# Optimization experiments

Measured on AMD Instinct MI355X. Metric: run time of the kernel, lower is better.

The kernel has to match this reference:

```python
import jax, jax.numpy as jnp
import numpy as np

B, T, D, H = 4, 256, 256, 4
D2 = 2 * D
DH = D2 // H
SCALE = float(D) ** -0.5


def _swish(x):
    return x * jax.nn.sigmoid(x)


def setup_inputs():
    key = jax.random.key(0)
    ks = jax.random.split(key, 16)

    def w(k, shape, fan_in):
        return jax.random.normal(k, shape, dtype=jnp.float32) / np.float32(np.sqrt(fan_in))

    return {
        "x": jax.random.normal(ks[0], (B, T, D), dtype=jnp.float32),
        "ln_g": jnp.ones((D,), jnp.float32), "ln_b": jnp.zeros((D,), jnp.float32),
        "W_left": w(ks[1], (D2, D), D), "b_left": jnp.zeros((D2,), jnp.float32),
        "W_right": w(ks[2], (D2, D), D), "b_right": jnp.zeros((D2,), jnp.float32),
        "Wi": w(ks[3], (1, D2), D2), "bi": jnp.zeros((1,), jnp.float32),
        "Wf": w(ks[4], (1, D2), D2), "bf": jnp.zeros((1,), jnp.float32),
        "Wo": w(ks[5], (D2, D2), D2), "bo": jnp.zeros((D2,), jnp.float32),
        "Wq": w(ks[6], (H, DH, DH), DH),
        "Wk": w(ks[7], (H, DH, DH), DH),
        "Wv": w(ks[8], (H, DH, DH), DH),
        "conv_w": w(ks[9], (D2, D2, 4), D2 * 4), "conv_b": jnp.zeros((D2,), jnp.float32),
        "skip_W": w(ks[10], (D2, D2), D2),
        "gn_g": jnp.ones((D2,), jnp.float32), "gn_b": jnp.zeros((D2,), jnp.float32),
        "W_last": w(ks[11], (D, D2), D2), "b_last": jnp.zeros((D,), jnp.float32),
    }


def reference(x, ln_g, ln_b, W_left, b_left, W_right, b_right, Wi, bi, Wf, bf,
              Wo, bo, Wq, Wk, Wv, conv_w, conv_b, skip_W, gn_g, gn_b, W_last, b_last):
    # LayerNorm over last dim (eps=1e-5, torch default)
    mu = x.mean(-1, keepdims=True)
    var = x.var(-1, keepdims=True)
    x_norm = (x - mu) * jax.lax.rsqrt(var + 1e-5) * ln_g + ln_b

    x_left = x_norm @ W_left.T + b_left          # (B,T,D2)
    x_right = x_norm @ W_right.T + b_right       # (B,T,D2)

    # causal conv1d: kernel 4, left pad 3
    xc = jnp.transpose(x_left, (0, 2, 1))        # (B,C,T)
    yc = jax.lax.conv_general_dilated(xc, conv_w, (1,), [(3, 0)],
                                      dimension_numbers=("NCH", "OIH", "NCH"))
    x_trans = _swish(jnp.transpose(yc + conv_b[None, :, None], (0, 2, 1)))  # (B,T,D2)

    def bd(z, W):  # block-diagonal linear, W: (H, out_h, in_h)
        zr = z.reshape(B, T, H, DH)
        return jnp.einsum("bthi,hoi->btho", zr, W).reshape(B, T, D2)

    # precompute all per-step projections (hoist GEMMs out of the scan)
    i_bar = x_left @ Wi.T + bi                   # (B,T,1)
    f_bar = x_left @ Wf.T + bf                   # (B,T,1)
    o = jax.nn.sigmoid(x_left @ Wo.T + bo)       # (B,T,D2)
    q = bd(x_trans, Wq)
    k = SCALE * bd(x_trans, Wk)
    v = bd(x_left, Wv)

    xs = tuple(jnp.swapaxes(a, 0, 1) for a in (i_bar, f_bar, q, k, v))  # (T,B,...)
    c0 = jnp.zeros((B, D2, D2), x.dtype)
    n0 = jnp.zeros((B, D2), x.dtype)
    m0 = jnp.zeros((B, 1), x.dtype)

    def step(carry, xs_t):
        c, n, m = carry
        ib, fb, qt, kt, vt = xs_t
        m_next = jnp.maximum(fb + m, ib)
        i_g = jnp.exp(ib - m_next)               # (B,1)
        f_g = jnp.exp(fb + m - m_next)           # (B,1)
        c_next = f_g[..., None] * c + i_g[..., None] * (vt[:, :, None] * kt[:, None, :])
        n_next = f_g * n + i_g * kt
        cq = jnp.einsum("bde,be->bd", c_next, qt)
        denom = jnp.maximum(jnp.abs(jnp.sum(n_next * qt, -1, keepdims=True)), 1.0)
        return (c_next, n_next, m_next), cq / (denom + 1e-8)

    _, h_bar = jax.lax.scan(step, (c0, n0, m0), xs)
    h_seq = o * jnp.swapaxes(h_bar, 0, 1)        # (B,T,D2), output gate applied per step

    # GroupNorm on (B, C, T): normalize per (batch, group) over C/G and T
    z = h_seq.reshape(B, T, H, DH)
    mu_g = z.mean(axis=(1, 3), keepdims=True)
    var_g = z.var(axis=(1, 3), keepdims=True)
    zn = ((z - mu_g) * jax.lax.rsqrt(var_g + 1e-5)).reshape(B, T, D2)
    h_gn = zn * gn_g + gn_b + x_trans @ skip_W.T

    h = h_gn * _swish(x_right)
    return h @ W_last.T + b_last + x
```

## Files before the change

kernel.cpp:

```cpp
#include <hip/hip_runtime.h>
#include <hip/hip_bf16.h>
#include <cstdint>

#define Bz 4
#define Tz 256
#define Dz 256
#define D2z 512
#define Hz 4
#define DHz 128
#define BT (Bz*Tz)

__device__ __forceinline__ float dot4(float4 a, float4 b){
  return a.x*b.x + a.y*b.y + a.z*b.z + a.w*b.w;
}
__device__ __forceinline__ float sigmoidf_(float z){ return 1.f/(1.f+__expf(-z)); }
__device__ __forceinline__ float4 fma4(float4 a, float4 w, float s){
  a.x += w.x*s; a.y += w.y*s; a.z += w.z*s; a.w += w.w*s; return a;
}
__device__ __forceinline__ float4 add4(float4 a, float4 b){
  a.x+=b.x; a.y+=b.y; a.z+=b.z; a.w+=b.w; return a;
}

__global__ void __launch_bounds__(512,2) k_pre(
    const float* __restrict__ Wo, const float* __restrict__ SW,
    const float* __restrict__ Wl, const float* __restrict__ Wq,
    const float* __restrict__ Wk, const float* __restrict__ Wv,
    const float* __restrict__ CW,
    float* __restrict__ Wot, float* __restrict__ SWt, float* __restrict__ WLt,
    float* __restrict__ Wqt, float* __restrict__ Wkt, float* __restrict__ Wvt,
    float* __restrict__ CWt,
    const float* __restrict__ x, const float* __restrict__ lg,
    const float* __restrict__ lb, const float* __restrict__ WL,
    const float* __restrict__ bL, const float* __restrict__ WR,
    const float* __restrict__ bR,
    const float* __restrict__ Wi, const float* __restrict__ bi,
    const float* __restrict__ Wf, const float* __restrict__ bf,
    float* __restrict__ xl, float* __restrict__ xr,
    float* __restrict__ ibp, float* __restrict__ fbp){
  __shared__ __align__(16) float smem[4224];
  int bid = blockIdx.x, tid = threadIdx.x;
  if (bid < 208){
    float (*ts)[65] = (float(*)[65])smem;
    const float* src; float* dst; int O,K,to,tk;
    if (bid<64){ src=Wo; dst=Wot; O=512;K=512; to=bid>>3; tk=bid&7; }
    else if (bid<128){ int r=bid-64; src=SW; dst=SWt; O=512;K=512; to=r>>3; tk=r&7; }
    else if (bid<160){ int r=bid-128; src=Wl; dst=WLt; O=256;K=512; to=r>>3; tk=r&7; }
    else {
      int r=bid-160; int m=r>>4; int rr=r&15; int h=rr>>2; int s=rr&3;
      src=(m==0?Wq:m==1?Wk:Wv) + h*16384;
      dst=(m==0?Wqt:m==1?Wkt:Wvt) + h*16384;
      O=128; K=128; to=s>>1; tk=s&1;
    }
    int lk=tid&63, ro=tid>>6;
    #pragma unroll
    for(int p=0;p<8;p++) ts[p*8+ro][lk] = src[(size_t)(to*64+p*8+ro)*K + tk*64+lk];
    __syncthreads();
    #pragma unroll
    for(int p=0;p<8;p++) dst[(size_t)(tk*64+p*8+ro)*O + to*64+lk] = ts[lk][p*8+ro];
  } else if (bid < 464){
    float4 (*t4)[33] = (float4(*)[33])smem;
    int r = bid-208; int to=r>>4, tk=r&15;
    const float4* src4=(const float4*)CW; float4* dst4=(float4*)CWt;
    int li=tid&31, ro=tid>>5;
    #pragma unroll
    for(int p=0;p<2;p++) t4[p*16+ro][li] = src4[(size_t)(to*32+p*16+ro)*512 + tk*32+li];
    __syncthreads();
    #pragma unroll
    for(int p=0;p<2;p++) dst4[(size_t)(tk*32+p*16+ro)*512 + to*32+li] = t4[li][p*16+ro];
  } else {
    float (*xs)[Dz] = (float(*)[Dz])smem;
    float (*rif)[4][8] = (float(*)[4][8])(smem + 8*Dz);
    int wbid = bid-464;
    int r0 = (wbid&127)*8; int oh = wbid>>7;
    ((float4*)&xs[0][0])[tid] = ((const float4*)(x + (size_t)r0*Dz))[tid];
    __syncthreads();
    int w = tid>>6, lane = tid&63;
    float a0 = xs[w][lane],     a1 = xs[w][lane+64];
    float a2 = xs[w][lane+128], a3 = xs[w][lane+192];
    float s  = a0+a1+a2+a3;
    float s2 = a0*a0+a1*a1+a2*a2+a3*a3;
    #pragma unroll
    for (int off=1; off<64; off<<=1){ s += __shfl_xor(s, off); s2 += __shfl_xor(s2, off); }
    float mu = s*(1.f/Dz);
    float rs = rsqrtf(s2*(1.f/Dz)-mu*mu+1e-5f);
    xs[w][lane]     = (a0-mu)*rs*lg[lane]    +lb[lane];
    xs[w][lane+64]  = (a1-mu)*rs*lg[lane+64] +lb[lane+64];
    xs[w][lane+128] = (a2-mu)*rs*lg[lane+128]+lb[lane+128];
    xs[w][lane+192] = (a3-mu)*rs*lg[lane+192]+lb[lane+192];
    __syncthreads();
    int which = tid>>8;
    int o = oh*256 + (tid&255);
    float acc[8]={0,0,0,0,0,0,0,0};
    const float* WM = which ? WR : WL;
    const float4* wm4 = (const float4*)(WM + (size_t)o*Dz);
    #pragma unroll 2
    for (int k4=0;k4<Dz/4;k4++){
      float4 wv=wm4[k4];
      #pragma unroll
      for(int tt=0;tt<8;tt++) acc[tt] += dot4(wv, ((const float4*)xs[tt])[k4]);
    }
    if (which==0){
      float blv=bL[o], wi_o=Wi[o], wf_o=Wf[o];
      float pi[8], pf[8];
      #pragma unroll
      for(int tt=0;tt<8;tt++){
        float xlv = acc[tt]+blv;
        xl[(size_t)(r0+tt)*D2z+o]=xlv;
        pi[tt]=xlv*wi_o; pf[tt]=xlv*wf_o;
      }
      #pragma unroll
      for(int off=1;off<64;off<<=1){
        #pragma unroll
        for(int tt=0;tt<8;tt++){ pi[tt]+=__shfl_xor(pi[tt],off); pf[tt]+=__shfl_xor(pf[tt],off); }
      }
      if(lane==0){
        #pragma unroll
        for(int tt=0;tt<8;tt++){ rif[0][w][tt]=pi[tt]; rif[1][w][tt]=pf[tt]; }
      }
    } else {
      float brv=bR[o];
      #pragma unroll
      for(int tt=0;tt<8;tt++) xr[(size_t)(r0+tt)*D2z+o]=acc[tt]+brv;
    }
    __syncthreads();
    if(tid<16){
      int r=tid&7, which2=tid>>3;
      float sv=0.f;
      #pragma unroll
      for(int ww=0;ww<4;ww++) sv+=rif[which2][ww][r];
      float bias = (oh==0) ? (which2==0 ? bi[0] : bf[0]) : 0.f;
      (which2==0 ? ibp : fbp)[oh*BT + r0 + r] = sv + bias;
    }
  }
}

__global__ void __launch_bounds__(256,2) k_mid(
    const float* __restrict__ xl, const float* __restrict__ CWt,
    const float* __restrict__ cb, float* __restrict__ xt,
    const float* __restrict__ Wot, const float* __restrict__ bo,
    const float* __restrict__ Wvt, float* __restrict__ og, float* __restrict__ vv,
    const float* __restrict__ ibp, const float* __restrict__ fbp,
    float* __restrict__ G, float* __restrict__ Mx){
  __shared__ __align__(16) float smem[9728];
  int bid = blockIdx.x, tid = threadIdx.x;
  if (bid < 512){
    float (*xs)[D2z] = (float(*)[D2z])smem;
    int tile = bid&63, o0 = (bid>>6)*64;
    int b = tile>>4; int t0 = (tile&15)*16;
    for(int idx=tid; idx<19*(D2z/4); idx+=256){
      int j = idx>>7, k4 = idx&127;
      int t = t0-3+j;
      float4 v = (t>=0) ? ((const float4*)(xl + (size_t)((b<<8)+t)*D2z))[k4]
                        : make_float4(0.f,0.f,0.f,0.f);
      ((float4*)xs[j])[k4]=v;
    }
    __syncthreads();
    int ol = tid&63, ch = tid>>6;
    int o = o0 + ol, ic0 = ch*128;
    float acc[16];
    #pragma unroll
    for(int tt=0;tt<16;tt++) acc[tt]=0.f;
    const float4* w4 = (const float4*)CWt + o;
    for(int i=0;i<128;i+=4){
      int ig = ic0+i;
      float4 w0=w4[(size_t)(ig+0)*512], w1=w4[(size_t)(ig+1)*512];
      float4 w2=w4[(size_t)(ig+2)*512], w3=w4[(size_t)(ig+3)*512];
      float4 xr4[19];
      #pragma unroll
      for(int j=0;j<19;j++) xr4[j]=*(const float4*)&xs[j][ig];
      #pragma unroll
      for(int tt=0;tt<16;tt++){
        acc[tt] += w0.x*xr4[tt].x + w0.y*xr4[tt+1].x + w0.z*xr4[tt+2].x + w0.w*xr4[tt+3].x
                 + w1.x*xr4[tt].y + w1.y*xr4[tt+1].y + w1.z*xr4[tt+2].y + w1.w*xr4[tt+3].y
                 + w2.x*xr4[tt].z + w2.y*xr4[tt+1].z + w2.z*xr4[tt+2].z + w2.w*xr4[tt+3].z
                 + w3.x*xr4[tt].w + w3.y*xr4[tt+1].w + w3.z*xr4[tt+2].w + w3.w*xr4[tt+3].w;
      }
    }
    __syncthreads();
    float (*red)[64][17] = (float(*)[64][17])smem;
    #pragma unroll
    for(int tt=0;tt<16;tt++) red[ch][ol][tt]=acc[tt];
    __syncthreads();
    for(int idx=tid; idx<1024; idx+=256){
      int oo = idx&63, t = idx>>6;
      float y = red[0][oo][t]+red[1][oo][t]+red[2][oo][t]+red[3][oo][t] + cb[o0+oo];
      xt[(size_t)((b<<8)+t0+t)*D2z + o0+oo] = y*sigmoidf_(y);
    }
  } else if (bid < 1024){
    float (*xs)[D2z] = (float(*)[D2z])smem;
    float4 (*red)[4][64] = (float4(*)[4][64])(smem + 2048);
    int wbid = bid-512;
    int r0=(wbid&255)*4; int oh=wbid>>8;
    for(int idx=tid;idx<512;idx+=256)
      ((float4*)&xs[0][0])[idx]=((const float4*)(xl+(size_t)r0*D2z))[idx];
    __syncthreads();
    int ol=tid&63, ch=tid>>6;
    {
      float4 a0={0,0,0,0},a1={0,0,0,0},a2={0,0,0,0},a3={0,0,0,0};
      const float4* wp=(const float4*)Wot + (size_t)ch*16384 + (oh*64+ol);
      #pragma unroll 2
      for(int kq=0;kq<32;kq++){
        int k=ch*128+kq*4;
        float4 w0=wp[(kq*4+0)*128], w1=wp[(kq*4+1)*128], w2=wp[(kq*4+2)*128], w3=wp[(kq*4+3)*128];
        float4 x0=*(const float4*)&xs[0][k];
        float4 x1=*(const float4*)&xs[1][k];
        float4 x2=*(const float4*)&xs[2][k];
        float4 x3=*(const float4*)&xs[3][k];
        a0=fma4(fma4(fma4(fma4(a0,w0,x0.x),w1,x0.y),w2,x0.z),w3,x0.w);
        a1=fma4(fma4(fma4(fma4(a1,w0,x1.x),w1,x1.y),w2,x1.z),w3,x1.w);
        a2=fma4(fma4(fma4(fma4(a2,w0,x2.x),w1,x2.y),w2,x2.z),w3,x2.w);
        a3=fma4(fma4(fma4(fma4(a3,w0,x3.x),w1,x3.y),w2,x3.z),w3,x3.w);
      }
      red[ch][0][ol]=a0; red[ch][1][ol]=a1; red[ch][2][ol]=a2; red[ch][3][ol]=a3;
    }
    __syncthreads();
    {
      float4 s=add4(add4(red[0][ch][ol],red[1][ch][ol]),add4(red[2][ch][ol],red[3][ch][ol]));
      float4 bb=((const float4*)bo)[oh*64+ol];
      s.x=sigmoidf_(s.x+bb.x); s.y=sigmoidf_(s.y+bb.y);
      s.z=sigmoidf_(s.z+bb.z); s.w=sigmoidf_(s.w+bb.w);
      ((float4*)(og+(size_t)(r0+ch)*D2z))[oh*64+ol]=s;
    }
    __syncthreads();
    {
      int h = oh*2 + (ol>>5), odq = ol&31;
      float4 v0={0,0,0,0},v1={0,0,0,0},v2={0,0,0,0},v3={0,0,0,0};
      const float4* wv=(const float4*)Wvt + (size_t)h*4096 + (size_t)(ch*32)*32 + odq;
      int xoff = h*128 + ch*32;
      #pragma unroll 2
      for(int iq=0;iq<8;iq++){
        float4 w0=wv[(iq*4+0)*32], w1=wv[(iq*4+1)*32], w2=wv[(iq*4+2)*32], w3=wv[(iq*4+3)*32];
        float4 x0=*(const float4*)&xs[0][xoff+iq*4];
        float4 x1=*(const float4*)&xs[1][xoff+iq*4];
        float4 x2=*(const float4*)&xs[2][xoff+iq*4];
        float4 x3=*(const float4*)&xs[3][xoff+iq*4];
        v0=fma4(fma4(fma4(fma4(v0,w0,x0.x),w1,x0.y),w2,x0.z),w3,x0.w);
        v1=fma4(fma4(fma4(fma4(v1,w0,x1.x),w1,x1.y),w2,x1.z),w3,x1.w);
        v2=fma4(fma4(fma4(fma4(v2,w0,x2.x),w1,x2.y),w2,x2.z),w3,x2.w);
        v3=fma4(fma4(fma4(fma4(v3,w0,x3.x),w1,x3.y),w2,x3.z),w3,x3.w);
      }
      red[ch][0][ol]=v0; red[ch][1][ol]=v1; red[ch][2][ol]=v2; red[ch][3][ol]=v3;
    }
    __syncthreads();
    {
      float4 vs=add4(add4(red[0][ch][ol],red[1][ch][ol]),add4(red[2][ch][ol],red[3][ch][ol]));
      ((float4*)(vv+(size_t)(r0+ch)*D2z))[oh*64+ol]=vs;
    }
  } else {
    float* buf = smem;
    int b = bid-1024, t = tid;
    float f = fbp[b*Tz + t] + fbp[BT + b*Tz + t];
    float ibv = ibp[b*Tz + t] + ibp[BT + b*Tz + t];
    buf[t] = f; __syncthreads();
    float v = f;
    for (int off=1; off<Tz; off<<=1){
      float add = (t >= off) ? buf[t-off] : 0.f;
      __syncthreads();
      v += add; buf[t] = v;
      __syncthreads();
    }
    float F = v;
    float g = ibv - F;
    G[b*Tz+t] = g;
    buf[t] = g; __syncthreads();
    v = g;
    for (int off=1; off<Tz; off<<=1){
      float other = (t >= off) ? buf[t-off] : -3.4e38f;
      __syncthreads();
      v = fmaxf(v, other); buf[t] = v;
      __syncthreads();
    }
    Mx[b*Tz+t] = fmaxf(v, 0.f);
  }
}

__global__ void __launch_bounds__(256,2) k_qks(const float* __restrict__ xt,
    const float* __restrict__ SWt, const float* __restrict__ Wqt,
    const float* __restrict__ Wkt,
    float* __restrict__ qq, float* __restrict__ kk, float* __restrict__ sk){
  __shared__ __align__(16) float smem[6144];
  float (*xs)[D2z] = (float(*)[D2z])smem;
  float4 (*red)[4][64] = (float4(*)[4][64])(smem + 2048);
  int r0=blockIdx.x*4; int oh=blockIdx.y; int tid=threadIdx.x;
  for(int idx=tid;idx<512;idx+=256)
    ((float4*)&xs[0][0])[idx]=((const float4*)(xt+(size_t)r0*D2z))[idx];
  __syncthreads();
  int ol=tid&63, ch=tid>>6;
  {
    float4 s0={0,0,0,0},s1={0,0,0,0},s2={0,0,0,0},s3={0,0,0,0};
    const float4* wp=(const float4*)SWt + (size_t)ch*16384 + (oh*64+ol);
    #pragma unroll 2
    for(int kq=0;kq<32;kq++){
      int k=ch*128+kq*4;
      float4 w0=wp[(kq*4+0)*128], w1=wp[(kq*4+1)*128], w2=wp[(kq*4+2)*128], w3=wp[(kq*4+3)*128];
      float4 x0=*(const float4*)&xs[0][k];
      float4 x1=*(const float4*)&xs[1][k];
      float4 x2=*(const float4*)&xs[2][k];
      float4 x3=*(const float4*)&xs[3][k];
      s0=fma4(fma4(fma4(fma4(s0,w0,x0.x),w1,x0.y),w2,x0.z),w3,x0.w);
      s1=fma4(fma4(fma4(fma4(s1,w0,x1.x),w1,x1.y),w2,x1.z),w3,x1.w);
      s2=fma4(fma4(fma4(fma4(s2,w0,x2.x),w1,x2.y),w2,x2.z),w3,x2.w);
      s3=fma4(fma4(fma4(fma4(s3,w0,x3.x),w1,x3.y),w2,x3.z),w3,x3.w);
    }
    red[ch][0][ol]=s0; red[ch][1][ol]=s1; red[ch][2][ol]=s2; red[ch][3][ol]=s3;
  }
  __syncthreads();
  {
    float4 sv=add4(add4(red[0][ch][ol],red[1][ch][ol]),add4(red[2][ch][ol],red[3][ch][ol]));
    ((float4*)(sk+(size_t)(r0+ch)*D2z))[oh*64+ol]=sv;
  }
  __syncthreads();
  int h = oh*2 + (ol>>5), odq = ol&31;
  int xoff = h*128 + ch*32;
  {
    float4 q0={0,0,0,0},q1={0,0,0,0},q2={0,0,0,0},q3={0,0,0,0};
    const float4* wq=(const float4*)Wqt + (size_t)h*4096 + (size_t)(ch*32)*32 + odq;
    #pragma unroll 2
    for(int iq=0;iq<8;iq++){
      float4 w0=wq[(iq*4+0)*32], w1=wq[(iq*4+1)*32], w2=wq[(iq*4+2)*32], w3=wq[(iq*4+3)*32];
      float4 x0=*(const float4*)&xs[0][xoff+iq*4];
      float4 x1=*(const float4*)&xs[1][xoff+iq*4];
      float4 x2=*(const float4*)&xs[2][xoff+iq*4];
      float4 x3=*(const float4*)&xs[3][xoff+iq*4];
      q0=fma4(fma4(fma4(fma4(q0,w0,x0.x),w1,x0.y),w2,x0.z),w3,x0.w);
      q1=fma4(fma4(fma4(fma4(q1,w0,x1.x),w1,x1.y),w2,x1.z),w3,x1.w);
      q2=fma4(fma4(fma4(fma4(q2,w0,x2.x),w1,x2.y),w2,x2.z),w3,x2.w);
      q3=fma4(fma4(fma4(fma4(q3,w0,x3.x),w1,x3.y),w2,x3.z),w3,x3.w);
    }
    red[ch][0][ol]=q0; red[ch][1][ol]=q1; red[ch][2][ol]=q2; red[ch][3][ol]=q3;
  }
  __syncthreads();
  {
    float4 qv=add4(add4(red[0][ch][ol],red[1][ch][ol]),add4(red[2][ch][ol],red[3][ch][ol]));
    ((float4*)(qq+(size_t)(r0+ch)*D2z))[oh*64+ol]=qv;
  }
  __syncthreads();
  {
    float4 k0={0,0,0,0},k1={0,0,0,0},k2={0,0,0,0},k3={0,0,0,0};
    const float4* wk=(const float4*)Wkt + (size_t)h*4096 + (size_t)(ch*32)*32 + odq;
    #pragma unroll 2
    for(int iq=0;iq<8;iq++){
      float4 w0=wk[(iq*4+0)*32], w1=wk[(iq*4+1)*32], w2=wk[(iq*4+2)*32], w3=wk[(iq*4+3)*32];
      float4 x0=*(const float4*)&xs[0][xoff+iq*4];
      float4 x1=*(const float4*)&xs[1][xoff+iq*4];
      float4 x2=*(const float4*)&xs[2][xoff+iq*4];
      float4 x3=*(const float4*)&xs[3][xoff+iq*4];
      k0=fma4(fma4(fma4(fma4(k0,w0,x0.x),w1,x0.y),w2,x0.z),w3,x0.w);
      k1=fma4(fma4(fma4(fma4(k1,w0,x1.x),w1,x1.y),w2,x1.z),w3,x1.w);
      k2=fma4(fma4(fma4(fma4(k2,w0,x2.x),w1,x2.y),w2,x2.z),w3,x2.w);
      k3=fma4(fma4(fma4(fma4(k3,w0,x3.x),w1,x3.y),w2,x3.z),w3,x3.w);
    }
    red[ch][0][ol]=k0; red[ch][1][ol]=k1; red[ch][2][ol]=k2; red[ch][3][ol]=k3;
  }
  __syncthreads();
  {
    float4 kv=add4(add4(red[0][ch][ol],red[1][ch][ol]),add4(red[2][ch][ol],red[3][ch][ol]));
    kv.x*=0.0625f; kv.y*=0.0625f; kv.z*=0.0625f; kv.w*=0.0625f;
    ((float4*)(kk+(size_t)(r0+ch)*D2z))[oh*64+ol]=kv;
  }
}

#define TTa 4
__global__ void __launch_bounds__(256) k_attn(
    const float* __restrict__ qq, const float* __restrict__ kk,
    const float* __restrict__ vv, const float* __restrict__ og,
    const float* __restrict__ G, const float* __restrict__ Mx,
    float* __restrict__ hs, float* __restrict__ gnp){
  int b  = blockIdx.y;
  int t0 = blockIdx.x * TTa;
  int tid = threadIdx.x;
  __shared__ float Qs[TTa][D2z];
  __shared__ float Ps[TTa][Tz];
  __shared__ float Gs[Tz];
  __shared__ float inv_d[TTa];
  __shared__ float mxs[TTa];

  const float* qb = qq + ((size_t)b*Tz + t0)*D2z;
  for (int idx=tid; idx<TTa*D2z/4; idx+=256)
    ((float4*)&Qs[0][0])[idx] = ((const float4*)qb)[idx];
  Gs[tid] = G[b*Tz + tid];
  if (tid < TTa) mxs[tid] = Mx[b*Tz + t0 + tid];
  __syncthreads();

  int s = tid;
  int smax = t0 + TTa - 1;
  {
    float acc[TTa] = {0,0,0,0};
    if (s <= smax){
      const float4* kp = (const float4*)(kk + ((size_t)b*Tz + s)*D2z);
      for (int k4=0; k4<D2z/4; k4++){
        float4 kv = kp[k4];
        #pragma unroll
        for (int tt=0; tt<TTa; tt++){
          float4 qv = ((const float4*)Qs[tt])[k4];
          acc[tt] += dot4(kv,qv);
        }
      }
    }
    float g = Gs[s];
    #pragma unroll
    for (int tt=0; tt<TTa; tt++){
      int t = t0 + tt;
      Ps[tt][s] = (s <= t) ? acc[tt] * __expf(g - mxs[tt]) : 0.f;
    }
  }
  __syncthreads();
  {
    int wv = tid >> 6, lane = tid & 63;
    int tt = wv;
    float ssum = Ps[tt][lane] + Ps[tt][lane+64] + Ps[tt][lane+128] + Ps[tt][lane+192];
    #pragma unroll
    for (int off=1; off<64; off<<=1) ssum += __shfl_xor(ssum, off);
    if (lane==0) inv_d[tt] = 1.f / (fmaxf(fabsf(ssum), 1.f) + 1e-8f);
  }
  __syncthreads();
  {
    int c0 = tid, c1 = tid + 256;
    float a0[TTa]={0,0,0,0}, a1[TTa]={0,0,0,0};
    const float* vb = vv + (size_t)b*Tz*D2z;
    for (int s2=0; s2<=smax; s2+=4){
      float4 pr[TTa];
      #pragma unroll
      for (int tt=0; tt<TTa; tt++) pr[tt] = *(const float4*)&Ps[tt][s2];
      #pragma unroll
      for (int j=0; j<4; j++){
        int sj = s2 + j;
        float v0 = vb[(size_t)sj*D2z + c0];
        float v1 = vb[(size_t)sj*D2z + c1];
        #pragma unroll
        for (int tt=0; tt<TTa; tt++){
          float p = ((const float*)&pr[tt])[j];
          a0[tt] += p*v0; a1[tt] += p*v1;
        }
      }
    }
    float s0=0.f,q0=0.f,s1=0.f,q1=0.f;
    #pragma unroll
    for (int tt=0; tt<TTa; tt++){
      size_t row = (size_t)b*Tz + t0 + tt;
      float id = inv_d[tt];
      float h0 = og[row*D2z + c0] * a0[tt] * id;
      float h1 = og[row*D2z + c1] * a1[tt] * id;
      hs[row*D2z + c0] = h0;
      hs[row*D2z + c1] = h1;
      s0+=h0; q0+=h0*h0; s1+=h1; q1+=h1*h1;
    }
    #pragma unroll
    for (int off=1; off<64; off<<=1){
      s0+=__shfl_xor(s0,off); q0+=__shfl_xor(q0,off);
      s1+=__shfl_xor(s1,off); q1+=__shfl_xor(q1,off);
    }
    if ((tid&63)==0){
      int wv=tid>>6, tile=blockIdx.x, half=wv&1;
      int g0=b*4+(wv>>1), g1=b*4+2+(wv>>1);
      float* p0 = gnp + ((size_t)(g0*64+tile)*2+half)*2;
      p0[0]=s0; p0[1]=q0;
      float* p1 = gnp + ((size_t)(g1*64+tile)*2+half)*2;
      p1[0]=s1; p1[1]=q1;
    }
  }
}

__global__ void __launch_bounds__(512,2) k_final(const float* __restrict__ hs,
    const float* __restrict__ gnp,
    const float* __restrict__ gng, const float* __restrict__ gnb,
    const float* __restrict__ sk, const float* __restrict__ xr,
    const float* __restrict__ WLt, const float* __restrict__ bl,
    const float* __restrict__ x, float* __restrict__ out){
  __shared__ __align__(16) float smem[8192];
  __shared__ float ls[16];
  __shared__ float gst[8];
  int r0=blockIdx.x*4; int b=r0>>8; int tid=threadIdx.x;
  {
    int w=tid>>6, lane=tid&63;
    int g=b*4+(w>>1), half=w&1;
    const float* p = gnp + ((size_t)(g*64+lane)*2 + half)*2;
    float s=p[0], q=p[1];
    #pragma unroll
    for(int off=1;off<64;off<<=1){ s+=__shfl_xor(s,off); q+=__shfl_xor(q,off); }
    if(lane==0){ ls[w*2]=s; ls[w*2+1]=q; }
  }
  __syncthreads();
  if(tid<4){
    float S = ls[4*tid]   + ls[4*tid+2];
    float S2= ls[4*tid+1] + ls[4*tid+3];
    float mu=S*(1.f/(Tz*DHz));
    float var=S2*(1.f/(Tz*DHz))-mu*mu;
    gst[tid]=mu; gst[4+tid]=rsqrtf(fmaxf(var,0.f)+1e-5f);
  }
  __syncthreads();
  float (*hm)[D2z] = (float(*)[D2z])smem;
  for(int idx=tid;idx<4*D2z;idx+=512){
    int tt=idx>>9,c=idx&511;
    size_t row=r0+tt;
    int gl=c>>7;
    float v=hs[row*D2z+c];
    float hg=(v-gst[gl])*gst[4+gl]*gng[c]+gnb[c]+sk[row*D2z+c];
    float xv=xr[row*D2z+c];
    hm[tt][c]=hg*(xv*sigmoidf_(xv));
  }
  __syncthreads();
  int ol=tid&63, ch=tid>>6;
  float4 a0={0,0,0,0},a1={0,0,0,0},a2={0,0,0,0},a3={0,0,0,0};
  const float4* wp=(const float4*)WLt + (size_t)(ch*64)*64 + ol;
  #pragma unroll 2
  for(int kq=0;kq<16;kq++){
    int k=ch*64+kq*4;
    float4 w0=wp[(kq*4+0)*64], w1=wp[(kq*4+1)*64], w2=wp[(kq*4+2)*64], w3=wp[(kq*4+3)*64];
    float4 x0=*(const float4*)&hm[0][k];
    float4 x1=*(const float4*)&hm[1][k];
    float4 x2=*(const float4*)&hm[2][k];
    float4 x3=*(const float4*)&hm[3][k];
    a0=fma4(fma4(fma4(fma4(a0,w0,x0.x),w1,x0.y),w2,x0.z),w3,x0.w);
    a1=fma4(fma4(fma4(fma4(a1,w0,x1.x),w1,x1.y),w2,x1.z),w3,x1.w);
    a2=fma4(fma4(fma4(fma4(a2,w0,x2.x),w1,x2.y),w2,x2.z),w3,x2.w);
    a3=fma4(fma4(fma4(fma4(a3,w0,x3.x),w1,x3.y),w2,x3.z),w3,x3.w);
  }
  __syncthreads();
  float4 (*red)[4][64] = (float4(*)[4][64])smem;
  red[ch][0][ol]=a0; red[ch][1][ol]=a1; red[ch][2][ol]=a2; red[ch][3][ol]=a3;
  __syncthreads();
  if(tid<256){
    int tt=tid>>6, oo=tid&63;
    float4 sv={0,0,0,0};
    #pragma unroll
    for(int c2=0;c2<8;c2++) sv=add4(sv,red[c2][tt][oo]);
    float4 bb=((const float4*)bl)[oo];
    float4 xv=((const float4*)(x+(size_t)(r0+tt)*Dz))[oo];
    sv.x+=bb.x+xv.x; sv.y+=bb.y+xv.y; sv.z+=bb.z+xv.z; sv.w+=bb.w+xv.w;
    ((float4*)(out+(size_t)(r0+tt)*Dz))[oo]=sv;
  }
}

extern "C" void kernel_launch(void* const* d_in, const int* in_sizes, int n_in,
                              void* d_out, int out_size, void* d_ws, size_t ws_size,
                              hipStream_t stream) {
  (void)in_sizes; (void)n_in; (void)out_size; (void)ws_size;
  const float* x      = (const float*)d_in[0];
  const float* ln_g   = (const float*)d_in[1];
  const float* ln_b   = (const float*)d_in[2];
  const float* W_left = (const float*)d_in[3];
  const float* b_left = (const float*)d_in[4];
  const float* W_right= (const float*)d_in[5];
  const float* b_right= (const float*)d_in[6];
  const float* Wi     = (const float*)d_in[7];
  const float* bi     = (const float*)d_in[8];
  const float* Wf     = (const float*)d_in[9];
  const float* bf     = (const float*)d_in[10];
  const float* Wo     = (const float*)d_in[11];
  const float* bo     = (const float*)d_in[12];
  const float* Wq     = (const float*)d_in[13];
  const float* Wk     = (const float*)d_in[14];
  const float* Wv     = (const float*)d_in[15];
  const float* conv_w = (const float*)d_in[16];
  const float* conv_b = (const float*)d_in[17];
  const float* skip_W = (const float*)d_in[18];
  const float* gn_g   = (const float*)d_in[19];
  const float* gn_b   = (const float*)d_in[20];
  const float* W_last = (const float*)d_in[21];
  const float* b_last = (const float*)d_in[22];
  float* out = (float*)d_out;

  float* ws = (float*)d_ws;
  float* Wot  = ws;
  float* xl   = ws + 262144;
  float* xr   = ws + 786432;
  float* xt   = ws + 1310720;
  float* og   = ws + 1835008;
  float* vv   = ws + 2359296;
  float* qq   = ws + 2883584;
  float* kk   = ws + 3407872;
  float* sk   = ws + 3932160;
  float* hs   = ws + 4456448;
  float* ibp  = ws + 4980736;
  float* fbp  = ws + 4982784;
  float* Gd   = ws + 4984864;
  float* Mxd  = ws + 4985888;
  float* SWt  = ws + 4986912;
  float* WLt  = ws + 5249056;
  float* Wqt  = ws + 5380128;
  float* Wkt  = ws + 5445664;
  float* Wvt  = ws + 5511200;
  float* CWt  = ws + 5576736;
  float* gnp  = ws + 6625312;

  k_pre   <<<720, 512, 0, stream>>>(Wo, skip_W, W_last, Wq, Wk, Wv, conv_w,
                                    Wot, SWt, WLt, Wqt, Wkt, Wvt, CWt,
                                    x, ln_g, ln_b, W_left, b_left, W_right, b_right,
                                    Wi, bi, Wf, bf, xl, xr, ibp, fbp);
  k_mid   <<<1028, 256, 0, stream>>>(xl, CWt, conv_b, xt, Wot, bo, Wvt, og, vv,
                                     ibp, fbp, Gd, Mxd);
  k_qks   <<<dim3(BT/4, 2), 256, 0, stream>>>(xt, SWt, Wqt, Wkt, qq, kk, sk);
  k_attn  <<<dim3(Tz/TTa, Bz), 256, 0, stream>>>(qq, kk, vv, og, Gd, Mxd, hs, gnp);
  k_final <<<BT/4, 512, 0, stream>>>(hs, gnp, gn_g, gn_b, sk, xr, WLt, b_last, x, out);
}
```

Measured before the change: 157.9 us.

## Read activations straight from global memory instead of staging in LDS

Gives the x_left buffer a per-batch zero-padded layout: four zero rows are written by k_pre, so the causal conv no longer needs bounds checks. The conv, gate/value, q/k/skip and attention kernels now read their activation rows directly from global memory (relying on L1/L2 and broadcast) instead of copying them into shared memory first. This removes a shared-memory fill and barrier per block and shrinks the LDS footprint, which may allow more blocks per CU. The cost is repeated uncached-in-LDS global loads per thread, and workspace offsets are shifted to fit the padding.

```diff
diff --git a/kernel.cpp b/kernel.cpp
--- a/kernel.cpp
+++ b/kernel.cpp
@@ -9,6 +9,8 @@
 #define Hz 4
 #define DHz 128
 #define BT (Bz*Tz)
+#define XLS 133120
+#define XLP 4
 
 __device__ __forceinline__ float dot4(float4 a, float4 b){
   return a.x*b.x + a.y*b.y + a.z*b.z + a.w*b.w;
@@ -40,6 +42,13 @@
   __shared__ __align__(16) float smem[4224];
   int bid = blockIdx.x, tid = threadIdx.x;
   if (bid < 208){
+    if (bid==0){
+      float4 z = make_float4(0.f,0.f,0.f,0.f);
+      for(int i=tid;i<2048;i+=512){
+        int b4=i>>9, idx=i&511;
+        ((float4*)xl)[(size_t)b4*(XLS/4) + idx] = z;
+      }
+    }
     float (*ts)[65] = (float(*)[65])smem;
     const float* src; float* dst; int O,K,to,tk;
     if (bid<64){ src=Wo; dst=Wot; O=512;K=512; to=bid>>3; tk=bid&7; }
@@ -72,6 +81,7 @@
     float (*rif)[4][8] = (float(*)[4][8])(smem + 8*Dz);
     int wbid = bid-464;
     int r0 = (wbid&127)*8; int oh = wbid>>7;
+    int bb2 = r0>>8, tb2 = r0&255;
     ((float4*)&xs[0][0])[tid] = ((const float4*)(x + (size_t)r0*Dz))[tid];
     __syncthreads();
     int w = tid>>6, lane = tid&63;
@@ -105,7 +115,7 @@
       #pragma unroll
       for(int tt=0;tt<8;tt++){
         float xlv = acc[tt]+blv;
-        xl[(size_t)(r0+tt)*D2z+o]=xlv;
+        xl[(size_t)bb2*XLS + (size_t)(XLP+tb2+tt)*D2z + o] = xlv;
         pi[tt]=xlv*wi_o; pf[tt]=xlv*wf_o;
       }
       #pragma unroll
@@ -141,22 +151,15 @@
     const float* __restrict__ Wvt, float* __restrict__ og, float* __restrict__ vv,
     const float* __restrict__ ibp, const float* __restrict__ fbp,
     float* __restrict__ G, float* __restrict__ Mx){
-  __shared__ __align__(16) float smem[9728];
+  __shared__ __align__(16) float smem[4352];
   int bid = blockIdx.x, tid = threadIdx.x;
   if (bid < 512){
-    float (*xs)[D2z] = (float(*)[D2z])smem;
+    float (*red)[64][17] = (float(*)[64][17])smem;
     int tile = bid&63, o0 = (bid>>6)*64;
     int b = tile>>4; int t0 = (tile&15)*16;
-    for(int idx=tid; idx<19*(D2z/4); idx+=256){
-      int j = idx>>7, k4 = idx&127;
-      int t = t0-3+j;
-      float4 v = (t>=0) ? ((const float4*)(xl + (size_t)((b<<8)+t)*D2z))[k4]
-                        : make_float4(0.f,0.f,0.f,0.f);
-      ((float4*)xs[j])[k4]=v;
-    }
-    __syncthreads();
     int ol = tid&63, ch = tid>>6;
     int o = o0 + ol, ic0 = ch*128;
+    const float* xb = xl + (size_t)b*XLS + (size_t)(t0+1)*D2z + ic0;
     float acc[16];
     #pragma unroll
     for(int tt=0;tt<16;tt++) acc[tt]=0.f;
@@ -167,7 +170,7 @@
       float4 w2=w4[(size_t)(ig+2)*512], w3=w4[(size_t)(ig+3)*512];
       float4 xr4[19];
       #pragma unroll
-      for(int j=0;j<19;j++) xr4[j]=*(const float4*)&xs[j][ig];
+      for(int j=0;j<19;j++) xr4[j]=*(const float4*)&xb[(size_t)j*D2z + i];
       #pragma unroll
       for(int tt=0;tt<16;tt++){
         acc[tt] += w0.x*xr4[tt].x + w0.y*xr4[tt+1].x + w0.z*xr4[tt+2].x + w0.w*xr4[tt+3].x
@@ -176,8 +179,6 @@
                  + w3.x*xr4[tt].w + w3.y*xr4[tt+1].w + w3.z*xr4[tt+2].w + w3.w*xr4[tt+3].w;
       }
     }
-    __syncthreads();
-    float (*red)[64][17] = (float(*)[64][17])smem;
     #pragma unroll
     for(int tt=0;tt<16;tt++) red[ch][ol][tt]=acc[tt];
     __syncthreads();
@@ -187,13 +188,11 @@
       xt[(size_t)((b<<8)+t0+t)*D2z + o0+oo] = y*sigmoidf_(y);
     }
   } else if (bid < 1024){
-    float (*xs)[D2z] = (float(*)[D2z])smem;
-    float4 (*red)[4][64] = (float4(*)[4][64])(smem + 2048);
+    float4 (*red)[4][64] = (float4(*)[4][64])smem;
     int wbid = bid-512;
     int r0=(wbid&255)*4; int oh=wbid>>8;
-    for(int idx=tid;idx<512;idx+=256)
-      ((float4*)&xs[0][0])[idx]=((const float4*)(xl+(size_t)r0*D2z))[idx];
-    __syncthreads();
+    int b = r0>>8, trow = r0&255;
+    const float* xp = xl + (size_t)b*XLS + (size_t)(XLP+trow)*D2z;
     int ol=tid&63, ch=tid>>6;
     {
       float4 a0={0,0,0,0},a1={0,0,0,0},a2={0,0,0,0},a3={0,0,0,0};
@@ -202,10 +201,10 @@
       for(int kq=0;kq<32;kq++){
         int k=ch*128+kq*4;
         float4 w0=wp[(kq*4+0)*128], w1=wp[(kq*4+1)*128], w2=wp[(kq*4+2)*128], w3=wp[(kq*4+3)*128];
-        float4 x0=*(const float4*)&xs[0][k];
-        float4 x1=*(const float4*)&xs[1][k];
-        float4 x2=*(const float4*)&xs[2][k];
-        float4 x3=*(const float4*)&xs[3][k];
+        float4 x0=*(const float4*)&xp[k];
+        float4 x1=*(const float4*)&xp[D2z+k];
+        float4 x2=*(const float4*)&xp[2*D2z+k];
+        float4 x3=*(const float4*)&xp[3*D2z+k];
         a0=fma4(fma4(fma4(fma4(a0,w0,x0.x),w1,x0.y),w2,x0.z),w3,x0.w);
         a1=fma4(fma4(fma4(fma4(a1,w0,x1.x),w1,x1.y),w2,x1.z),w3,x1.w);
         a2=fma4(fma4(fma4(fma4(a2,w0,x2.x),w1,x2.y),w2,x2.z),w3,x2.w);
@@ -230,10 +229,11 @@
       #pragma unroll 2
       for(int iq=0;iq<8;iq++){
         float4 w0=wv[(iq*4+0)*32], w1=wv[(iq*4+1)*32], w2=wv[(iq*4+2)*32], w3=wv[(iq*4+3)*32];
-        float4 x0=*(const float4*)&xs[0][xoff+iq*4];
-        float4 x1=*(const float4*)&xs[1][xoff+iq*4];
-        float4 x2=*(const float4*)&xs[2][xoff+iq*4];
-        float4 x3=*(const float4*)&xs[3][xoff+iq*4];
+        int k=xoff+iq*4;
+        float4 x0=*(const float4*)&xp[k];
+        float4 x1=*(const float4*)&xp[D2z+k];
+        float4 x2=*(const float4*)&xp[2*D2z+k];
+        float4 x3=*(const float4*)&xp[3*D2z+k];
         v0=fma4(fma4(fma4(fma4(v0,w0,x0.x),w1,x0.y),w2,x0.z),w3,x0.w);
         v1=fma4(fma4(fma4(fma4(v1,w0,x1.x),w1,x1.y),w2,x1.z),w3,x1.w);
         v2=fma4(fma4(fma4(fma4(v2,w0,x2.x),w1,x2.y),w2,x2.z),w3,x2.w);
@@ -278,13 +278,10 @@
     const float* __restrict__ SWt, const float* __restrict__ Wqt,
     const float* __restrict__ Wkt,
     float* __restrict__ qq, float* __restrict__ kk, float* __restrict__ sk){
-  __shared__ __align__(16) float smem[6144];
-  float (*xs)[D2z] = (float(*)[D2z])smem;
-  float4 (*red)[4][64] = (float4(*)[4][64])(smem + 2048);
+  __shared__ __align__(16) float smem[4096];
+  float4 (*red)[4][64] = (float4(*)[4][64])smem;
   int r0=blockIdx.x*4; int oh=blockIdx.y; int tid=threadIdx.x;
-  for(int idx=tid;idx<512;idx+=256)
-    ((float4*)&xs[0][0])[idx]=((const float4*)(xt+(size_t)r0*D2z))[idx];
-  __syncthreads();
+  const float* xp = xt + (size_t)r0*D2z;
   int ol=tid&63, ch=tid>>6;
   {
     float4 s0={0,0,0,0},s1={0,0,0,0},s2={0,0,0,0},s3={0,0,0,0};
@@ -293,10 +290,10 @@
     for(int kq=0;kq<32;kq++){
       int k=ch*128+kq*4;
       float4 w0=wp[(kq*4+0)*128], w1=wp[(kq*4+1)*128], w2=wp[(kq*4+2)*128], w3=wp[(kq*4+3)*128];
-      float4 x0=*(const float4*)&xs[0][k];
-      float4 x1=*(const float4*)&xs[1][k];
-      float4 x2=*(const float4*)&xs[2][k];
-      float4 x3=*(const float4*)&xs[3][k];
+      float4 x0=*(const float4*)&xp[k];
+      float4 x1=*(const float4*)&xp[D2z+k];
+      float4 x2=*(const float4*)&xp[2*D2z+k];
+      float4 x3=*(const float4*)&xp[3*D2z+k];
       s0=fma4(fma4(fma4(fma4(s0,w0,x0.x),w1,x0.y),w2,x0.z),w3,x0.w);
       s1=fma4(fma4(fma4(fma4(s1,w0,x1.x),w1,x1.y),w2,x1.z),w3,x1.w);
       s2=fma4(fma4(fma4(fma4(s2,w0,x2.x),w1,x2.y),w2,x2.z),w3,x2.w);
@@ -318,10 +315,11 @@
     #pragma unroll 2
     for(int iq=0;iq<8;iq++){
       float4 w0=wq[(iq*4+0)*32], w1=wq[(iq*4+1)*32], w2=wq[(iq*4+2)*32], w3=wq[(iq*4+3)*32];
-      float4 x0=*(const float4*)&xs[0][xoff+iq*4];
-      float4 x1=*(const float4*)&xs[1][xoff+iq*4];
-      float4 x2=*(const float4*)&xs[2][xoff+iq*4];
-      float4 x3=*(const float4*)&xs[3][xoff+iq*4];
+      int k=xoff+iq*4;
+      float4 x0=*(const float4*)&xp[k];
+      float4 x1=*(const float4*)&xp[D2z+k];
+      float4 x2=*(const float4*)&xp[2*D2z+k];
+      float4 x3=*(const float4*)&xp[3*D2z+k];
       q0=fma4(fma4(fma4(fma4(q0,w0,x0.x),w1,x0.y),w2,x0.z),w3,x0.w);
       q1=fma4(fma4(fma4(fma4(q1,w0,x1.x),w1,x1.y),w2,x1.z),w3,x1.w);
       q2=fma4(fma4(fma4(fma4(q2,w0,x2.x),w1,x2.y),w2,x2.z),w3,x2.w);
@@ -341,10 +339,11 @@
     #pragma unroll 2
     for(int iq=0;iq<8;iq++){
       float4 w0=wk[(iq*4+0)*32], w1=wk[(iq*4+1)*32], w2=wk[(iq*4+2)*32], w3=wk[(iq*4+3)*32];
-      float4 x0=*(const float4*)&xs[0][xoff+iq*4];
-      float4 x1=*(const float4*)&xs[1][xoff+iq*4];
-      float4 x2=*(const float4*)&xs[2][xoff+iq*4];
-      float4 x3=*(const float4*)&xs[3][xoff+iq*4];
+      int k=xoff+iq*4;
+      float4 x0=*(const float4*)&xp[k];
+      float4 x1=*(const float4*)&xp[D2z+k];
+      float4 x2=*(const float4*)&xp[2*D2z+k];
+      float4 x3=*(const float4*)&xp[3*D2z+k];
       k0=fma4(fma4(fma4(fma4(k0,w0,x0.x),w1,x0.y),w2,x0.z),w3,x0.w);
       k1=fma4(fma4(fma4(fma4(k1,w0,x1.x),w1,x1.y),w2,x1.z),w3,x1.w);
       k2=fma4(fma4(fma4(fma4(k2,w0,x2.x),w1,x2.y),w2,x2.z),w3,x2.w);
@@ -369,16 +368,11 @@
   int b  = blockIdx.y;
   int t0 = blockIdx.x * TTa;
   int tid = threadIdx.x;
-  __shared__ float Qs[TTa][D2z];
   __shared__ float Ps[TTa][Tz];
-  __shared__ float Gs[Tz];
   __shared__ float inv_d[TTa];
   __shared__ float mxs[TTa];
 
   const float* qb = qq + ((size_t)b*Tz + t0)*D2z;
-  for (int idx=tid; idx<TTa*D2z/4; idx+=256)
-    ((float4*)&Qs[0][0])[idx] = ((const float4*)qb)[idx];
-  Gs[tid] = G[b*Tz + tid];
   if (tid < TTa) mxs[tid] = Mx[b*Tz + t0 + tid];
   __syncthreads();
 
@@ -392,12 +386,12 @@
         float4 kv = kp[k4];
         #pragma unroll
         for (int tt=0; tt<TTa; tt++){
-          float4 qv = ((const float4*)Qs[tt])[k4];
+          float4 qv = *(const float4*)&qb[(size_t)tt*D2z + k4*4];
           acc[tt] += dot4(kv,qv);
         }
       }
     }
-    float g = Gs[s];
+    float g = G[b*Tz + s];
     #pragma unroll
     for (int tt=0; tt<TTa; tt++){
       int t = t0 + tt;
@@ -564,25 +558,25 @@
   float* ws = (float*)d_ws;
   float* Wot  = ws;
   float* xl   = ws + 262144;
-  float* xr   = ws + 786432;
-  float* xt   = ws + 1310720;
-  float* og   = ws + 1835008;
-  float* vv   = ws + 2359296;
-  float* qq   = ws + 2883584;
-  float* kk   = ws + 3407872;
-  float* sk   = ws + 3932160;
-  float* hs   = ws + 4456448;
-  float* ibp  = ws + 4980736;
-  float* fbp  = ws + 4982784;
-  float* Gd   = ws + 4984864;
-  float* Mxd  = ws + 4985888;
-  float* SWt  = ws + 4986912;
-  float* WLt  = ws + 5249056;
-  float* Wqt  = ws + 5380128;
-  float* Wkt  = ws + 5445664;
-  float* Wvt  = ws + 5511200;
-  float* CWt  = ws + 5576736;
-  float* gnp  = ws + 6625312;
+  float* xr   = ws + 794624;
+  float* xt   = ws + 1318912;
+  float* og   = ws + 1843200;
+  float* vv   = ws + 2367488;
+  float* qq   = ws + 2891776;
+  float* kk   = ws + 3416064;
+  float* sk   = ws + 3940352;
+  float* hs   = ws + 4464640;
+  float* ibp  = ws + 4988928;
+  float* fbp  = ws + 4990976;
+  float* Gd   = ws + 4993024;
+  float* Mxd  = ws + 4994048;
+  float* SWt  = ws + 4995072;
+  float* WLt  = ws + 5257216;
+  float* Wqt  = ws + 5388288;
+  float* Wkt  = ws + 5453824;
+  float* Wvt  = ws + 5519360;
+  float* CWt  = ws + 5584896;
+  float* gnp  = ws + 6633472;
 
   k_pre   <<<720, 512, 0, stream>>>(Wo, skip_W, W_last, Wq, Wk, Wv, conv_w,
                                     Wot, SWt, WLt, Wqt, Wkt, Wvt, CWt,
```

Result: slower. 179.4 us (+13.6%).
